# Kernel tuning notes

Hardware: AMD Instinct MI355X
Metric: run time of the kernel (lower is better)

## Reference

```python
import jax, jax.numpy as jnp
import numpy as np
import math

HIDDEN = 768
HEADS = 12
HEAD_DIM = HIDDEN // HEADS
B, S = 2, 4096


def setup_inputs() -> dict:
    key = jax.random.key(0)
    ks = jax.random.split(key, 12)
    scale = 1.0 / math.sqrt(HIDDEN)
    inp = {
        "key": jax.random.normal(ks[0], (B, S, HIDDEN), jnp.float32),
        "value": jax.random.normal(ks[1], (B, S, HIDDEN), jnp.float32),
        "query": jax.random.normal(ks[2], (B, S, HIDDEN), jnp.float32),
        "mask": jnp.zeros((B, 1, S, S), jnp.float32),
        # weights stored as [in, out] so projection is x @ W + b
        "Wq": jax.random.normal(ks[3], (HIDDEN, HIDDEN), jnp.float32) * scale,
        "bq": jnp.zeros((HIDDEN,), jnp.float32),
        "Wk": jax.random.normal(ks[4], (HIDDEN, HIDDEN), jnp.float32) * scale,
        "bk": jnp.zeros((HIDDEN,), jnp.float32),
        "Wv": jax.random.normal(ks[5], (HIDDEN, HIDDEN), jnp.float32) * scale,
        "bv": jnp.zeros((HIDDEN,), jnp.float32),
        "Wo": jax.random.normal(ks[6], (HIDDEN, HIDDEN), jnp.float32) * scale,
        "bo": jnp.zeros((HIDDEN,), jnp.float32),
    }
    return inp


def reference(key, value, query, mask, Wq, bq, Wk, bk, Wv, bv, Wo, bo):
    b, s, h = key.shape
    def proj(x, W, bias):
        # [b,s,h] -> [b, heads, s, head_dim]
        y = jnp.dot(x, W) + bias
        return y.reshape(b, s, HEADS, HEAD_DIM).transpose(0, 2, 1, 3)

    q = proj(query, Wq, bq)
    k = proj(key, Wk, bk)
    v = proj(value, Wv, bv)

    inv_sqrt_d = 1.0 / math.sqrt(float(HEAD_DIM))
    scores = jnp.einsum("bnqd,bnkd->bnqk", q, k) * inv_sqrt_d + mask
    probs = jax.nn.softmax(scores, axis=-1)  # dropout p=0.0 -> identity
    ctx = jnp.einsum("bnqk,bnkd->bnqd", probs, v)
    ctx = ctx.transpose(0, 2, 1, 3).reshape(b, s, h)
    return jnp.dot(ctx, Wo) + bo
```

## Files before the change

kernel.cpp:

```cpp
#include <hip/hip_runtime.h>
#include <hip/hip_bf16.h>
#include <math.h>

#define HID 768
#define NH 12
#define HD 64
#define BB 2
#define SS 4096
#define MM (BB*SS)

typedef unsigned short u16;
typedef __attribute__((ext_vector_type(8))) short short8;
typedef __attribute__((ext_vector_type(8))) unsigned short u16x8;
typedef __attribute__((ext_vector_type(4))) float f32x4;
typedef __attribute__((ext_vector_type(16))) float f32x16;

__device__ __forceinline__ u16 f2bf(float f) {
  union { float f; unsigned u; } v; v.f = f;
  return (u16)((v.u + 0x7fffu + ((v.u >> 16) & 1u)) >> 16);
}

__device__ __forceinline__ unsigned cvtpk(float lo, float hi) {
  unsigned r;
  asm("v_cvt_pk_bf16_f32 %0, %1, %2" : "=v"(r) : "v"(lo), "v"(hi));
  return r;
}

__device__ __forceinline__ short8 mk8(unsigned a, unsigned b, unsigned c, unsigned d) {
  union { unsigned u[4]; short8 s; } x;
  x.u[0] = a; x.u[1] = b; x.u[2] = c; x.u[3] = d;
  return x.s;
}

__device__ __forceinline__ void pls(unsigned &a, unsigned &b) {
  typedef __attribute__((ext_vector_type(2))) unsigned uv2;
  uv2 r = __builtin_amdgcn_permlane32_swap(a, b, false, false);
  a = r[0]; b = r[1];
}

__device__ __forceinline__ float swap_max(float x) {
  union { float f; unsigned u; } a, b; a.f = x; b.f = x;
  pls(a.u, b.u);
  return fmaxf(a.f, b.f);
}
__device__ __forceinline__ float swap_add(float x) {
  union { float f; unsigned u; } a, b; a.f = x; b.f = x;
  pls(a.u, b.u);
  return a.f + b.f;
}

#define C2F 0.18033688f
#define THR2 11.5415603f

__global__ void mask_scan(const uint4* __restrict__ m, long long n4, int* __restrict__ flag) {
  long long i = (long long)blockIdx.x * blockDim.x + threadIdx.x;
  long long stride = (long long)gridDim.x * blockDim.x;
  unsigned acc = 0;
  for (; i < n4; i += stride) {
    uint4 v = m[i];
    acc |= v.x | v.y | v.z | v.w;
  }
  if (__any(acc != 0)) {
    if ((threadIdx.x & 63) == 0) atomicOr(flag, 1);
  }
}

__global__ void w_transpose(const float* __restrict__ w0, const float* __restrict__ w1,
                            const float* __restrict__ w2, const float* __restrict__ w3,
                            u16* __restrict__ wt) {
  const float* W = (blockIdx.z == 0) ? w0 : (blockIdx.z == 1) ? w1 : (blockIdx.z == 2) ? w2 : w3;
  u16* Wt = wt + (size_t)blockIdx.z * HID * HID;
  __shared__ float tile[64][65];
  int kb = blockIdx.x * 64, nb = blockIdx.y * 64;
  int t = threadIdx.x;
  int r = t >> 2, cg = (t & 3) << 4;
  const float* src = W + (size_t)(kb + r) * HID + nb + cg;
#pragma unroll
  for (int i = 0; i < 4; i++) {
    float4 v = *(const float4*)(src + 4 * i);
    tile[r][cg + 4*i + 0] = v.x;
    tile[r][cg + 4*i + 1] = v.y;
    tile[r][cg + 4*i + 2] = v.z;
    tile[r][cg + 4*i + 3] = v.w;
  }
  __syncthreads();
  u16x8 a, b;
#pragma unroll
  for (int i = 0; i < 8; i++) a[i] = f2bf(tile[cg + i][r]);
#pragma unroll
  for (int i = 0; i < 8; i++) b[i] = f2bf(tile[cg + 8 + i][r]);
  u16* dst = Wt + (size_t)(nb + r) * HID + kb + cg;
  *(u16x8*)dst = a;
  *(u16x8*)(dst + 8) = b;
}

__global__ void v_transpose(const u16* __restrict__ v_bf, u16* __restrict__ vt_bf) {
  int bh = blockIdx.y, sb = blockIdx.x * 64;
  __shared__ u16 tile[64][72];
  const u16* src = v_bf + (size_t)bh * SS * HD;
  u16* dst = vt_bf + (size_t)bh * HD * SS;
  int t = threadIdx.x;
  int r = t >> 2, cg = (t & 3) << 4;
  *(u16x8*)(&tile[r][cg])     = *(const u16x8*)(src + (size_t)(sb + r) * HD + cg);
  *(u16x8*)(&tile[r][cg + 8]) = *(const u16x8*)(src + (size_t)(sb + r) * HD + cg + 8);
  __syncthreads();
  u16x8 a, b;
#pragma unroll
  for (int i = 0; i < 8; i++) a[i] = tile[cg + i][r];
#pragma unroll
  for (int i = 0; i < 8; i++) b[i] = tile[cg + 8 + i][r];
  *(u16x8*)(dst + (size_t)r * SS + sb + cg) = a;
  *(u16x8*)(dst + (size_t)r * SS + sb + cg + 8) = b;
}

__launch_bounds__(256)
__global__ void proj_qkv(const float* __restrict__ Xq, const float* __restrict__ Xk,
                         const float* __restrict__ Xv, const u16* __restrict__ wt,
                         const float* __restrict__ bq, const float* __restrict__ bk,
                         const float* __restrict__ bv,
                         u16* __restrict__ qo, u16* __restrict__ ko, u16* __restrict__ vo) {
  int which = blockIdx.z;
  const float* X   = which == 0 ? Xq : which == 1 ? Xk : Xv;
  const u16* Wt    = wt + (size_t)which * HID * HID;
  const float* bias = which == 0 ? bq : which == 1 ? bk : bv;
  u16* out         = which == 0 ? qo : which == 1 ? ko : vo;

  __shared__ u16 Al[128 * 40];
  __shared__ u16 Bl[128 * 40];
  int t = threadIdx.x;
  int mbase = blockIdx.x * 128, nbase = blockIdx.y * 128;
  int wid = t >> 6, lane = t & 63, g = lane >> 4, c = lane & 15;
  int wm = wid >> 1, wn = wid & 1;

  f32x4 acc[4][4];
#pragma unroll
  for (int i = 0; i < 4; i++)
#pragma unroll
    for (int j = 0; j < 4; j++) acc[i][j] = 0.0f;

  int ar = t >> 1, ac = (t & 1) << 4;
  const float* xrow = X  + (size_t)(mbase + ar) * HID + ac;
  const u16*   wrow = Wt + (size_t)(nbase + ar) * HID + ac;
  u16* adst = &Al[ar * 40 + ac];
  u16* bdst = &Bl[ar * 40 + ac];

  for (int k0 = 0; k0 < HID; k0 += 32) {
    float4 x0 = *(const float4*)(xrow + k0);
    float4 x1 = *(const float4*)(xrow + k0 + 4);
    float4 x2 = *(const float4*)(xrow + k0 + 8);
    float4 x3 = *(const float4*)(xrow + k0 + 12);
    u16x8 pa_, pb_;
    pa_[0]=f2bf(x0.x); pa_[1]=f2bf(x0.y); pa_[2]=f2bf(x0.z); pa_[3]=f2bf(x0.w);
    pa_[4]=f2bf(x1.x); pa_[5]=f2bf(x1.y); pa_[6]=f2bf(x1.z); pa_[7]=f2bf(x1.w);
    pb_[0]=f2bf(x2.x); pb_[1]=f2bf(x2.y); pb_[2]=f2bf(x2.z); pb_[3]=f2bf(x2.w);
    pb_[4]=f2bf(x3.x); pb_[5]=f2bf(x3.y); pb_[6]=f2bf(x3.z); pb_[7]=f2bf(x3.w);
    u16x8 w0 = *(const u16x8*)(wrow + k0);
    u16x8 w1 = *(const u16x8*)(wrow + k0 + 8);
    *(u16x8*)adst       = pa_;
    *(u16x8*)(adst + 8) = pb_;
    *(u16x8*)bdst       = w0;
    *(u16x8*)(bdst + 8) = w1;
    __syncthreads();
    short8 af[4], bfr[4];
#pragma unroll
    for (int i = 0; i < 4; i++)
      af[i] = *(const short8*)(&Al[(wm*64 + i*16 + c) * 40 + 8*g]);
#pragma unroll
    for (int i = 0; i < 4; i++)
      bfr[i] = *(const short8*)(&Bl[(wn*64 + i*16 + c) * 40 + 8*g]);
#pragma unroll
    for (int mi = 0; mi < 4; mi++)
#pragma unroll
      for (int ni = 0; ni < 4; ni++)
        acc[mi][ni] = __builtin_amdgcn_mfma_f32_16x16x32_bf16(af[mi], bfr[ni], acc[mi][ni], 0, 0, 0);
    __syncthreads();
  }
#pragma unroll
  for (int ni = 0; ni < 4; ni++) {
    int n = nbase + wn*64 + ni*16 + c;
    float bv_ = bias[n];
    int hh = n >> 6, dd = n & 63;
#pragma unroll
    for (int mi = 0; mi < 4; mi++)
#pragma unroll
      for (int j = 0; j < 4; j++) {
        int m = mbase + wm*64 + mi*16 + 4*g + j;
        int bidx = m >> 12, s_ = m & (SS - 1);
        out[(((size_t)bidx * NH + hh) * SS + s_) * HD + dd] = f2bf(acc[mi][ni][j] + bv_);
      }
  }
}

__launch_bounds__(256)
__global__ void proj_out(const u16* __restrict__ X, const u16* __restrict__ Wt,
                         const float* __restrict__ bias, float* __restrict__ out) {
  __shared__ u16 Al[128 * 40];
  __shared__ u16 Bl[128 * 40];
  int t = threadIdx.x;
  int mbase = blockIdx.x * 128, nbase = blockIdx.y * 128;
  int wid = t >> 6, lane = t & 63, g = lane >> 4, c = lane & 15;
  int wm = wid >> 1, wn = wid & 1;

  f32x4 acc[4][4];
#pragma unroll
  for (int i = 0; i < 4; i++)
#pragma unroll
    for (int j = 0; j < 4; j++) acc[i][j] = 0.0f;

  int ar = t >> 1, ac = (t & 1) << 4;
  const u16* xrow = X  + (size_t)(mbase + ar) * HID + ac;
  const u16* wrow = Wt + (size_t)(nbase + ar) * HID + ac;
  u16* adst = &Al[ar * 40 + ac];
  u16* bdst = &Bl[ar * 40 + ac];

  for (int k0 = 0; k0 < HID; k0 += 32) {
    u16x8 a0 = *(const u16x8*)(xrow + k0);
    u16x8 a1 = *(const u16x8*)(xrow + k0 + 8);
    u16x8 w0 = *(const u16x8*)(wrow + k0);
    u16x8 w1 = *(const u16x8*)(wrow + k0 + 8);
    *(u16x8*)adst       = a0;
    *(u16x8*)(adst + 8) = a1;
    *(u16x8*)bdst       = w0;
    *(u16x8*)(bdst + 8) = w1;
    __syncthreads();
    short8 af[4], bfr[4];
#pragma unroll
    for (int i = 0; i < 4; i++)
      af[i] = *(const short8*)(&Al[(wm*64 + i*16 + c) * 40 + 8*g]);
#pragma unroll
    for (int i = 0; i < 4; i++)
      bfr[i] = *(const short8*)(&Bl[(wn*64 + i*16 + c) * 40 + 8*g]);
#pragma unroll
    for (int mi = 0; mi < 4; mi++)
#pragma unroll
      for (int ni = 0; ni < 4; ni++)
        acc[mi][ni] = __builtin_amdgcn_mfma_f32_16x16x32_bf16(af[mi], bfr[ni], acc[mi][ni], 0, 0, 0);
    __syncthreads();
  }
#pragma unroll
  for (int ni = 0; ni < 4; ni++) {
    int n = nbase + wn*64 + ni*16 + c;
    float bv_ = bias[n];
#pragma unroll
    for (int mi = 0; mi < 4; mi++)
#pragma unroll
      for (int j = 0; j < 4; j++) {
        int m = mbase + wm*64 + mi*16 + 4*g + j;
        out[(size_t)m * HID + n] = acc[mi][ni][j] + bv_;
      }
  }
}

__launch_bounds__(256)
__global__ void attn(const u16* __restrict__ q_bf, const u16* __restrict__ k_bf,
                     const u16* __restrict__ vt_bf, const float* __restrict__ mask,
                     const int* __restrict__ flag, u16* __restrict__ ctx) {
  const int qb = blockIdx.x, bh = blockIdx.y;
  const int b = bh / NH, hh = bh - b * NH;
  const u16* Q  = q_bf  + (size_t)bh * SS * HD;
  const u16* K  = k_bf  + (size_t)bh * SS * HD;
  const u16* VT = vt_bf + (size_t)bh * HD * SS;
  const int t = threadIdx.x, wid = t >> 6, lane = t & 63;
  const int c5 = lane & 31, h2 = lane >> 5;
  const int qbase = qb * 128 + wid * 32;
  const int use_mask = *flag;

  __shared__ u16 KV[2 * 8192];

  short8 qf0, qf1, qf2, qf3;
  {
    const u16* qrow = Q + (size_t)(qbase + c5) * HD + 8 * h2;
    qf0 = *(const short8*)(qrow);
    qf1 = *(const short8*)(qrow + 16);
    qf2 = *(const short8*)(qrow + 32);
    qf3 = *(const short8*)(qrow + 48);
  }

  f32x16 o0, o1; o0 = 0.0f; o1 = 0.0f;
  float m2_run = -1e30f, l_run = 0.0f;

  const int sr = t >> 2, sq = t & 3;
  const int o_k0 = sr * 64 + (((2 * sq) ^ (sr & 7)) * 8);
  const u16* kp = K  + (size_t)sr * HD + sq * 16;
  const u16* vp = VT + (size_t)sr * SS + sq * 16;
  u16x8 rk0 = *(const u16x8*)kp, rk1 = *(const u16x8*)(kp + 8);
  u16x8 rv0 = *(const u16x8*)vp, rv1 = *(const u16x8*)(vp + 8);

  const int sw = c5 & 7;
  const int krow0 = c5 * 64, krow1 = (32 + c5) * 64;

  for (int tl = 0; tl < SS / 64; ++tl) {
    const int bufo = (tl & 1) * 8192;
    u16* kd = KV + bufo;
    *(u16x8*)(kd + o_k0)              = rk0;
    *(u16x8*)(kd + (o_k0 ^ 8))        = rk1;
    *(u16x8*)(kd + 4096 + o_k0)       = rv0;
    *(u16x8*)(kd + 4096 + (o_k0 ^ 8)) = rv1;
    if (tl < SS / 64 - 1) {
      kp += 64 * HD; vp += 64;
      rk0 = *(const u16x8*)kp; rk1 = *(const u16x8*)(kp + 8);
      rv0 = *(const u16x8*)vp; rv1 = *(const u16x8*)(vp + 8);
    }
    __syncthreads();
    const u16* Kb = KV + bufo;
    const u16* Vb = KV + bufo + 4096;

    f32x16 s0, s1; s0 = 0.0f; s1 = 0.0f;
    __builtin_amdgcn_s_setprio(1);
#pragma unroll
    for (int dc = 0; dc < 4; ++dc) {
      short8 qv = dc == 0 ? qf0 : dc == 1 ? qf1 : dc == 2 ? qf2 : qf3;
      short8 ka = *(const short8*)(Kb + krow0 + (((2 * dc + h2) ^ sw) * 8));
      s0 = __builtin_amdgcn_mfma_f32_32x32x16_bf16(ka, qv, s0, 0, 0, 0);
    }
#pragma unroll
    for (int dc = 0; dc < 4; ++dc) {
      short8 qv = dc == 0 ? qf0 : dc == 1 ? qf1 : dc == 2 ? qf2 : qf3;
      short8 ka = *(const short8*)(Kb + krow1 + (((2 * dc + h2) ^ sw) * 8));
      s1 = __builtin_amdgcn_mfma_f32_32x32x16_bf16(ka, qv, s1, 0, 0, 0);
    }
    __builtin_amdgcn_s_setprio(0);

    if (use_mask) {
      const float* mrow = mask + ((size_t)b * SS + (qbase + c5)) * SS + (size_t)tl * 64;
#pragma unroll
      for (int j = 0; j < 16; ++j) {
        const int row = (j & 3) + 8 * (j >> 2) + 4 * h2;
        s0[j] = fmaf(mrow[row],      8.0f, s0[j]);
        s1[j] = fmaf(mrow[32 + row], 8.0f, s1[j]);
      }
    }

    float rm = fmaxf(s0[0], s1[0]);
#pragma unroll
    for (int j = 1; j < 16; ++j) rm = fmaxf(rm, fmaxf(s0[j], s1[j]));
    const float pmax2 = swap_max(rm) * C2F;

    if (!__all(pmax2 <= m2_run + THR2)) {
      const float mn = fmaxf(m2_run, pmax2);
      const float ef = exp2f(m2_run - mn);
      m2_run = mn; l_run *= ef;
#pragma unroll
      for (int j = 0; j < 16; ++j) {
        const int row = (j & 3) + 8 * (j >> 2) + 4 * h2;
        const float eb = __shfl(ef, row);
        o0[j] *= eb; o1[j] *= eb;
      }
    }

    float ts = 0.0f;
#pragma unroll
    for (int j = 0; j < 16; ++j) { float p = exp2f(fmaf(s0[j], C2F, -m2_run)); s0[j] = p; ts += p; }
#pragma unroll
    for (int j = 0; j < 16; ++j) { float p = exp2f(fmaf(s1[j], C2F, -m2_run)); s1[j] = p; ts += p; }
    l_run += swap_add(ts);

    unsigned w00 = cvtpk(s0[0],  s0[1]),  w01 = cvtpk(s0[2],  s0[3]);
    unsigned w10 = cvtpk(s0[4],  s0[5]),  w11 = cvtpk(s0[6],  s0[7]);
    unsigned w20 = cvtpk(s0[8],  s0[9]),  w21 = cvtpk(s0[10], s0[11]);
    unsigned w30 = cvtpk(s0[12], s0[13]), w31 = cvtpk(s0[14], s0[15]);
    unsigned y00 = cvtpk(s1[0],  s1[1]),  y01 = cvtpk(s1[2],  s1[3]);
    unsigned y10 = cvtpk(s1[4],  s1[5]),  y11 = cvtpk(s1[6],  s1[7]);
    unsigned y20 = cvtpk(s1[8],  s1[9]),  y21 = cvtpk(s1[10], s1[11]);
    unsigned y30 = cvtpk(s1[12], s1[13]), y31 = cvtpk(s1[14], s1[15]);

    pls(w00, w10); pls(w01, w11);
    pls(w20, w30); pls(w21, w31);
    pls(y00, y10); pls(y01, y11);
    pls(y20, y30); pls(y21, y31);
    short8 p0 = mk8(w00, w01, w10, w11);
    short8 p1 = mk8(w20, w21, w30, w31);
    short8 p2 = mk8(y00, y01, y10, y11);
    short8 p3 = mk8(y20, y21, y30, y31);

    __builtin_amdgcn_s_setprio(1);
#pragma unroll
    for (int kc = 0; kc < 4; ++kc) {
      short8 pa = kc == 0 ? p0 : kc == 1 ? p1 : kc == 2 ? p2 : p3;
      short8 v0 = *(const short8*)(Vb + krow0 + (((2 * kc + h2) ^ sw) * 8));
      o0 = __builtin_amdgcn_mfma_f32_32x32x16_bf16(pa, v0, o0, 0, 0, 0);
      short8 v1 = *(const short8*)(Vb + krow1 + (((2 * kc + h2) ^ sw) * 8));
      o1 = __builtin_amdgcn_mfma_f32_32x32x16_bf16(pa, v1, o1, 0, 0, 0);
    }
    __builtin_amdgcn_s_setprio(0);
  }

  const float inv = 1.0f / l_run;
  u16* cbase = ctx + ((size_t)b * SS) * HID + hh * HD;
#pragma unroll
  for (int j = 0; j < 16; ++j) {
    const int row = (j & 3) + 8 * (j >> 2) + 4 * h2;
    const float ib = __shfl(inv, row);
    u16* crow = cbase + (size_t)(qbase + row) * HID;
    crow[c5]      = f2bf(o0[j] * ib);
    crow[32 + c5] = f2bf(o1[j] * ib);
  }
}

extern "C" void kernel_launch(void* const* d_in, const int* in_sizes, int n_in,
                              void* d_out, int out_size, void* d_ws, size_t ws_size,
                              hipStream_t stream) {
  (void)in_sizes; (void)n_in; (void)out_size; (void)ws_size;
  const float* key   = (const float*)d_in[0];
  const float* value = (const float*)d_in[1];
  const float* query = (const float*)d_in[2];
  const float* mask  = (const float*)d_in[3];
  const float* Wq = (const float*)d_in[4];
  const float* bq = (const float*)d_in[5];
  const float* Wk = (const float*)d_in[6];
  const float* bk = (const float*)d_in[7];
  const float* Wv = (const float*)d_in[8];
  const float* bv = (const float*)d_in[9];
  const float* Wo = (const float*)d_in[10];
  const float* bo = (const float*)d_in[11];

  char* ws = (char*)d_ws;
  const size_t WSZ = (size_t)HID * HID * 2;
  const size_t QSZ = (size_t)BB * NH * SS * HD * 2;
  u16* w_t   = (u16*)ws;
  u16* q_bf  = (u16*)(ws + 4*WSZ);
  u16* k_bf  = (u16*)(ws + 4*WSZ + QSZ);
  u16* v_bf  = (u16*)(ws + 4*WSZ + 2*QSZ);
  u16* vt_bf = (u16*)(ws + 4*WSZ + 3*QSZ);
  u16* ctx   = (u16*)(ws + 4*WSZ + 4*QSZ);
  int* flag  = (int*)(ws + 4*WSZ + 5*QSZ);

  hipMemsetAsync(flag, 0, 4, stream);
  mask_scan<<<2048, 256, 0, stream>>>((const uint4*)mask, (long long)BB*SS*SS/4, flag);
  w_transpose<<<dim3(12, 12, 4), 256, 0, stream>>>(Wq, Wk, Wv, Wo, w_t);
  proj_qkv<<<dim3(MM/128, HID/128, 3), 256, 0, stream>>>(query, key, value, w_t,
                                                         bq, bk, bv, q_bf, k_bf, v_bf);
  v_transpose<<<dim3(SS/64, BB*NH), 256, 0, stream>>>(v_bf, vt_bf);
  attn<<<dim3(SS/128, BB*NH), 256, 0, stream>>>(q_bf, k_bf, vt_bf, mask, flag, ctx);
  proj_out<<<dim3(MM/128, HID/128), 256, 0, stream>>>(ctx, w_t + 3*(size_t)HID*HID, bo,
                                                      (float*)d_out);
}
```

Before: 578.5 us.

## Compute softmax row sums via MFMA with ones, use raw exp/max3/rcp intrinsics

Replaces the per-lane scalar accumulation of softmax denominators with MFMA products of the bf16 probability tiles against a ones matrix, so the row sums land in the same layout as the output accumulator and need no cross-lane shuffle at the end. The row max now uses v_max3, exp2f is swapped for the raw v_exp_f32 instruction, the final divide becomes v_rcp_f32, and the projection's fp32-to-bf16 conversion uses the packed cvt instruction. The s_setprio hints around the MFMA blocks are removed. This adds four MFMAs per tile and sums bf16-rounded probabilities, which may change precision slightly.

```diff
diff --git a/kernel.cpp b/kernel.cpp
--- a/kernel.cpp
+++ b/kernel.cpp
@@ -26,12 +26,36 @@
   return r;
 }
 
+__device__ __forceinline__ float max3(float a, float b, float c) {
+  float r;
+  asm("v_max3_f32 %0, %1, %2, %3" : "=v"(r) : "v"(a), "v"(b), "v"(c));
+  return r;
+}
+
+__device__ __forceinline__ float exp2r(float x) {
+  float r;
+  asm("v_exp_f32 %0, %1" : "=v"(r) : "v"(x));
+  return r;
+}
+
+__device__ __forceinline__ float rcpr(float x) {
+  float r;
+  asm("v_rcp_f32 %0, %1" : "=v"(r) : "v"(x));
+  return r;
+}
+
 __device__ __forceinline__ short8 mk8(unsigned a, unsigned b, unsigned c, unsigned d) {
   union { unsigned u[4]; short8 s; } x;
   x.u[0] = a; x.u[1] = b; x.u[2] = c; x.u[3] = d;
   return x.s;
 }
 
+__device__ __forceinline__ u16x8 mku16(unsigned a, unsigned b, unsigned c, unsigned d) {
+  union { unsigned u[4]; u16x8 s; } x;
+  x.u[0] = a; x.u[1] = b; x.u[2] = c; x.u[3] = d;
+  return x.s;
+}
+
 __device__ __forceinline__ void pls(unsigned &a, unsigned &b) {
   typedef __attribute__((ext_vector_type(2))) unsigned uv2;
   uv2 r = __builtin_amdgcn_permlane32_swap(a, b, false, false);
@@ -42,11 +66,6 @@
   union { float f; unsigned u; } a, b; a.f = x; b.f = x;
   pls(a.u, b.u);
   return fmaxf(a.f, b.f);
-}
-__device__ __forceinline__ float swap_add(float x) {
-  union { float f; unsigned u; } a, b; a.f = x; b.f = x;
-  pls(a.u, b.u);
-  return a.f + b.f;
 }
 
 #define C2F 0.18033688f
@@ -149,11 +168,10 @@
     float4 x1 = *(const float4*)(xrow + k0 + 4);
     float4 x2 = *(const float4*)(xrow + k0 + 8);
     float4 x3 = *(const float4*)(xrow + k0 + 12);
-    u16x8 pa_, pb_;
-    pa_[0]=f2bf(x0.x); pa_[1]=f2bf(x0.y); pa_[2]=f2bf(x0.z); pa_[3]=f2bf(x0.w);
-    pa_[4]=f2bf(x1.x); pa_[5]=f2bf(x1.y); pa_[6]=f2bf(x1.z); pa_[7]=f2bf(x1.w);
-    pb_[0]=f2bf(x2.x); pb_[1]=f2bf(x2.y); pb_[2]=f2bf(x2.z); pb_[3]=f2bf(x2.w);
-    pb_[4]=f2bf(x3.x); pb_[5]=f2bf(x3.y); pb_[6]=f2bf(x3.z); pb_[7]=f2bf(x3.w);
+    u16x8 pa_ = mku16(cvtpk(x0.x, x0.y), cvtpk(x0.z, x0.w),
+                      cvtpk(x1.x, x1.y), cvtpk(x1.z, x1.w));
+    u16x8 pb_ = mku16(cvtpk(x2.x, x2.y), cvtpk(x2.z, x2.w),
+                      cvtpk(x3.x, x3.y), cvtpk(x3.z, x3.w));
     u16x8 w0 = *(const u16x8*)(wrow + k0);
     u16x8 w1 = *(const u16x8*)(wrow + k0 + 8);
     *(u16x8*)adst       = pa_;
@@ -276,8 +294,10 @@
     qf3 = *(const short8*)(qrow + 48);
   }
 
-  f32x16 o0, o1; o0 = 0.0f; o1 = 0.0f;
-  float m2_run = -1e30f, l_run = 0.0f;
+  f32x16 o0, o1, lacc; o0 = 0.0f; o1 = 0.0f; lacc = 0.0f;
+  float m2_run = -1e30f;
+
+  const short8 onesf = mk8(0x3F803F80u, 0x3F803F80u, 0x3F803F80u, 0x3F803F80u);
 
   const int sr = t >> 2, sq = t & 3;
   const int o_k0 = sr * 64 + (((2 * sq) ^ (sr & 7)) * 8);
@@ -306,7 +326,6 @@
     const u16* Vb = KV + bufo + 4096;
 
     f32x16 s0, s1; s0 = 0.0f; s1 = 0.0f;
-    __builtin_amdgcn_s_setprio(1);
 #pragma unroll
     for (int dc = 0; dc < 4; ++dc) {
       short8 qv = dc == 0 ? qf0 : dc == 1 ? qf1 : dc == 2 ? qf2 : qf3;
@@ -319,7 +338,6 @@
       short8 ka = *(const short8*)(Kb + krow1 + (((2 * dc + h2) ^ sw) * 8));
       s1 = __builtin_amdgcn_mfma_f32_32x32x16_bf16(ka, qv, s1, 0, 0, 0);
     }
-    __builtin_amdgcn_s_setprio(0);
 
     if (use_mask) {
       const float* mrow = mask + ((size_t)b * SS + (qbase + c5)) * SS + (size_t)tl * 64;
@@ -331,29 +349,33 @@
       }
     }
 
-    float rm = fmaxf(s0[0], s1[0]);
-#pragma unroll
-    for (int j = 1; j < 16; ++j) rm = fmaxf(rm, fmaxf(s0[j], s1[j]));
+    float a0 = max3(s0[0], s0[1], s0[2]),   a1 = max3(s0[3], s0[4], s0[5]);
+    float a2 = max3(s0[6], s0[7], s0[8]),   a3 = max3(s0[9], s0[10], s0[11]);
+    float a4 = max3(s0[12], s0[13], s0[14]);
+    float b0 = max3(s1[0], s1[1], s1[2]),   b1 = max3(s1[3], s1[4], s1[5]);
+    float b2 = max3(s1[6], s1[7], s1[8]),   b3 = max3(s1[9], s1[10], s1[11]);
+    float b4 = max3(s1[12], s1[13], s1[14]);
+    float c0 = max3(a0, a1, a2), c1 = max3(a3, a4, s0[15]);
+    float c2 = max3(b0, b1, b2), c3 = max3(b3, b4, s1[15]);
+    float rm = fmaxf(max3(c0, c1, c2), c3);
     const float pmax2 = swap_max(rm) * C2F;
 
     if (!__all(pmax2 <= m2_run + THR2)) {
       const float mn = fmaxf(m2_run, pmax2);
-      const float ef = exp2f(m2_run - mn);
-      m2_run = mn; l_run *= ef;
+      const float ef = exp2r(m2_run - mn);
+      m2_run = mn;
 #pragma unroll
       for (int j = 0; j < 16; ++j) {
         const int row = (j & 3) + 8 * (j >> 2) + 4 * h2;
         const float eb = __shfl(ef, row);
-        o0[j] *= eb; o1[j] *= eb;
+        o0[j] *= eb; o1[j] *= eb; lacc[j] *= eb;
       }
     }
 
-    float ts = 0.0f;
-#pragma unroll
-    for (int j = 0; j < 16; ++j) { float p = exp2f(fmaf(s0[j], C2F, -m2_run)); s0[j] = p; ts += p; }
-#pragma unroll
-    for (int j = 0; j < 16; ++j) { float p = exp2f(fmaf(s1[j], C2F, -m2_run)); s1[j] = p; ts += p; }
-    l_run += swap_add(ts);
+#pragma unroll
+    for (int j = 0; j < 16; ++j) s0[j] = exp2r(fmaf(s0[j], C2F, -m2_run));
+#pragma unroll
+    for (int j = 0; j < 16; ++j) s1[j] = exp2r(fmaf(s1[j], C2F, -m2_run));
 
     unsigned w00 = cvtpk(s0[0],  s0[1]),  w01 = cvtpk(s0[2],  s0[3]);
     unsigned w10 = cvtpk(s0[4],  s0[5]),  w11 = cvtpk(s0[6],  s0[7]);
@@ -373,7 +395,11 @@
     short8 p2 = mk8(y00, y01, y10, y11);
     short8 p3 = mk8(y20, y21, y30, y31);
 
-    __builtin_amdgcn_s_setprio(1);
+    lacc = __builtin_amdgcn_mfma_f32_32x32x16_bf16(p0, onesf, lacc, 0, 0, 0);
+    lacc = __builtin_amdgcn_mfma_f32_32x32x16_bf16(p1, onesf, lacc, 0, 0, 0);
+    lacc = __builtin_amdgcn_mfma_f32_32x32x16_bf16(p2, onesf, lacc, 0, 0, 0);
+    lacc = __builtin_amdgcn_mfma_f32_32x32x16_bf16(p3, onesf, lacc, 0, 0, 0);
+
 #pragma unroll
     for (int kc = 0; kc < 4; ++kc) {
       short8 pa = kc == 0 ? p0 : kc == 1 ? p1 : kc == 2 ? p2 : p3;
@@ -382,15 +408,13 @@
       short8 v1 = *(const short8*)(Vb + krow1 + (((2 * kc + h2) ^ sw) * 8));
       o1 = __builtin_amdgcn_mfma_f32_32x32x16_bf16(pa, v1, o1, 0, 0, 0);
     }
-    __builtin_amdgcn_s_setprio(0);
-  }
-
-  const float inv = 1.0f / l_run;
+  }
+
   u16* cbase = ctx + ((size_t)b * SS) * HID + hh * HD;
 #pragma unroll
   for (int j = 0; j < 16; ++j) {
     const int row = (j & 3) + 8 * (j >> 2) + 4 * h2;
-    const float ib = __shfl(inv, row);
+    const float ib = rcpr(lacc[j]);
     u16* crow = cbase + (size_t)(qbase + row) * HID;
     crow[c5]      = f2bf(o0[j] * ib);
     crow[32 + c5] = f2bf(o1[j] * ib);
```

Measured after the change: 516.5 us. 1.12x faster.
